# Kernel tuning notes

Measured on AMD Instinct MI355X. Metric: run time of the kernel, lower is better.

## Reference

```python
import jax, jax.numpy as jnp
import numpy as np

N = 50000   # nodes
R = 4       # relation groups
E = 800000  # nnz per relation adjacency
ED = 200000 # decoded edges
H = 128     # hidden_dim
L = 64      # latent_dim
DH = 64     # decoder_hidden_dim


def setup_inputs() -> dict:
    key = jax.random.key(0)
    ks = iter(jax.random.split(key, 64))
    def nrm(shape, scale=1.0):
        return jax.random.normal(next(ks), shape, dtype=jnp.float32) * scale
    inp = {}
    inp["x_process"] = nrm((N, 62))
    inp["x_file"] = nrm((N, 37))
    inp["x_network"] = nrm((N, 37))
    def lin(prefix, din, dout):
        s = 1.0 / np.sqrt(din)
        inp[prefix + "_Ws"] = nrm((dout, din), s)
        inp[prefix + "_bs"] = nrm((dout,), s)
        inp[prefix + "_Wr"] = nrm((R, dout, din), s)
        inp[prefix + "_br"] = nrm((R, dout), s)
    lin("p1", 62, H); lin("p2", H, L)
    lin("f1", 37, H); lin("f2", H, L)
    lin("n1", 37, H); lin("n2", H, L)
    inp["gate_W"] = nrm((3, L), 1.0 / np.sqrt(L))
    inp["gate_b"] = nrm((3,), 0.1)
    inp["dec_W1"] = nrm((DH, 4 * L), 1.0 / np.sqrt(4 * L))
    inp["dec_b1"] = nrm((DH,), 0.1)
    inp["dec_W2"] = nrm((1, DH), 1.0 / np.sqrt(DH))
    inp["dec_b2"] = nrm((1,), 0.1)
    inp["adj_rows"] = jax.random.randint(next(ks), (R, E), 0, N, dtype=jnp.int32)
    inp["adj_cols"] = jax.random.randint(next(ks), (R, E), 0, N, dtype=jnp.int32)
    inp["adj_vals"] = jax.random.uniform(next(ks), (R, E), dtype=jnp.float32) * 0.1
    inp["edge_src"] = jax.random.randint(next(ks), (ED,), 0, N, dtype=jnp.int32)
    inp["edge_dst"] = jax.random.randint(next(ks), (ED,), 0, N, dtype=jnp.int32)
    return inp


def reference(x_process, x_file, x_network,
              p1_Ws, p1_bs, p1_Wr, p1_br, p2_Ws, p2_bs, p2_Wr, p2_br,
              f1_Ws, f1_bs, f1_Wr, f1_br, f2_Ws, f2_bs, f2_Wr, f2_br,
              n1_Ws, n1_bs, n1_Wr, n1_br, n2_Ws, n2_bs, n2_Wr, n2_br,
              gate_W, gate_b, dec_W1, dec_b1, dec_W2, dec_b2,
              adj_rows, adj_cols, adj_vals, edge_src, edge_dst):
    def spmm(rows, cols, vals, x):  # A @ x, A in COO: out[row] += val * x[col]
        return jax.ops.segment_sum(vals[:, None] * x[cols], rows, num_segments=N)

    def rgcn_layer(x, Ws, bs, Wr, br):
        out = x @ Ws.T + bs  # self_linear
        for r in range(R):
            out = out + spmm(adj_rows[r], adj_cols[r], adj_vals[r], x) @ Wr[r].T + br[r]
        return out / float(R + 1)

    def encoder(x, W1s, b1s, W1r, b1r, W2s, b2s, W2r, b2r):
        h = jax.nn.relu(rgcn_layer(x, W1s, b1s, W1r, b1r))
        # dropout p=0.0 / eval mode -> identity
        return rgcn_layer(h, W2s, b2s, W2r, b2r)

    z_p = encoder(x_process, p1_Ws, p1_bs, p1_Wr, p1_br, p2_Ws, p2_bs, p2_Wr, p2_br)
    z_f = encoder(x_file, f1_Ws, f1_bs, f1_Wr, f1_br, f2_Ws, f2_bs, f2_Wr, f2_br)
    z_n = encoder(x_network, n1_Ws, n1_bs, n1_Wr, n1_br, n2_Ws, n2_bs, n2_Wr, n2_br)

    # gated multi-view fusion: three Linear(latent,1) gates -> softmax over views
    scores = jnp.stack([z_p @ gate_W[0] + gate_b[0],
                        z_f @ gate_W[1] + gate_b[1],
                        z_n @ gate_W[2] + gate_b[2]], axis=1)  # [N, 3]
    alpha = jax.nn.softmax(scores, axis=1)
    z = alpha[:, 0:1] * z_p + alpha[:, 1:2] * z_f + alpha[:, 2:3] * z_n  # [N, L]

    # mlp edge decoder
    zs = z[edge_src]
    zd = z[edge_dst]
    feats = jnp.concatenate([zs, zd, zs * zd, jnp.abs(zs - zd)], axis=1)  # [ED, 4L]
    hid = jax.nn.relu(feats @ dec_W1.T + dec_b1)
    logits = (hid @ dec_W2.T + dec_b2)[:, 0]  # [ED]
    return logits
```

## Files before the change

kernel.cpp:

```cpp
#include <hip/hip_runtime.h>

#define N_NODES 50000
#define R_REL   4
#define E_NNZ   800000
#define ED_EDGES 200000
#define H_DIM   128
#define L_DIM   64

#define RN_TOTAL (R_REL * N_NODES)
#define ETOT     (R_REL * E_NNZ)

#define EPB   8192
#define NB    391
#define RBK   196
#define KBK   (R_REL * RBK)
#define HTOT  (KBK * NB)
#define SCB   300
#define MAXB  6144

#define WS_RP    0u
#define WS_HIST  800256u
#define WS_BSUM  2026496u
#define WS_BIAS3 2028544u
#define WS_CV    2030592u
#define WS_YALL  27630720u
#define WS_TMP   27630720u
#define WS_UVZ   27630720u
#define WS_SF    53230720u
#define WS_SN    82830720u
#define WS_XALL  112430720u
#define WS_YSP   112430720u
#define WS_SP    131630720u
#define WS_HF    131630720u
#define WS_YSN   131630720u
#define WS_HN    157230720u
#define WS_HPR   188001536u
#define WS_YSF   188001536u
#define WS_Z     200801536u

__device__ __forceinline__ ushort f2bf(float f) {
    unsigned u = __float_as_uint(f);
    unsigned r = (u + 0x7fffu + ((u >> 16) & 1u)) >> 16;
    return (ushort)r;
}
__device__ __forceinline__ float bf2f(ushort u) {
    return __uint_as_float(((unsigned)u) << 16);
}

__global__ void cast_xall_kernel(const float* __restrict__ xp, const float* __restrict__ xf,
                                 const float* __restrict__ xn, ushort* __restrict__ xall) {
    int i = blockIdx.x * 256 + threadIdx.x;
    if (i >= N_NODES * 192) return;
    int node = i / 192, k = i - node * 192;
    float v = 0.f;
    if (k < 62) v = xp[node * 62 + k];
    else if (k >= 64 && k < 138) {
        int j = k - 64, d = j >> 1;
        v = (j & 1) ? xn[node * 37 + d] : xf[node * 37 + d];
    }
    xall[i] = f2bf(v);
}

__global__ void radix_hist_kernel(const int* __restrict__ rows, int* __restrict__ H) {
    __shared__ int hist[KBK];
    int blk = blockIdx.x, t = threadIdx.x;
    for (int i = t; i < KBK; i += 256) hist[i] = 0;
    __syncthreads();
    int base = blk * EPB;
    #pragma unroll 1
    for (int i = 0; i < EPB / 256; i++) {
        int g = base + i * 256 + t;
        if (g < ETOT) {
            int r = g / E_NNZ;
            atomicAdd(&hist[r * RBK + (rows[g] >> 8)], 1);
        }
    }
    __syncthreads();
    for (int i = t; i < KBK; i += 256) H[i * NB + blk] = hist[i];
}

__global__ void scan_part_kernel(const int* __restrict__ H, int* __restrict__ bsum) {
    __shared__ int red[256];
    int base = blockIdx.x * 1024, t = threadIdx.x;
    int s = 0;
    #pragma unroll
    for (int i = 0; i < 4; i++) {
        int idx = base + i * 256 + t;
        if (idx < HTOT) s += H[idx];
    }
    red[t] = s; __syncthreads();
    for (int d = 128; d > 0; d >>= 1) {
        if (t < d) red[t] += red[t + d];
        __syncthreads();
    }
    if (t == 0) bsum[blockIdx.x] = red[0];
}

__global__ void scan_bsum_kernel(int* __restrict__ bsum, int* __restrict__ rp) {
    __shared__ int sh[512];
    int t = threadIdx.x;
    int v = (t < SCB) ? bsum[t] : 0;
    sh[t] = v; __syncthreads();
    for (int d = 1; d < 512; d <<= 1) {
        int u = (t >= d) ? sh[t - d] : 0;
        __syncthreads();
        sh[t] += u;
        __syncthreads();
    }
    if (t < SCB) bsum[t] = sh[t] - v;
    if (t == 0) rp[RN_TOTAL] = ETOT;
}

__global__ void scan_final_kernel(int* __restrict__ H, const int* __restrict__ bsum) {
    __shared__ int sh[256];
    int base = blockIdx.x * 1024, t = threadIdx.x;
    int c[4]; int s = 0;
    #pragma unroll
    for (int i = 0; i < 4; i++) {
        int idx = base + t * 4 + i;
        c[i] = (idx < HTOT) ? H[idx] : 0;
        s += c[i];
    }
    sh[t] = s; __syncthreads();
    for (int d = 1; d < 256; d <<= 1) {
        int u = (t >= d) ? sh[t - d] : 0;
        __syncthreads();
        sh[t] += u;
        __syncthreads();
    }
    int off = bsum[blockIdx.x] + sh[t] - s;
    #pragma unroll
    for (int i = 0; i < 4; i++) {
        int idx = base + t * 4 + i;
        if (idx < HTOT) H[idx] = off;
        off += c[i];
    }
}

__global__ void radix_scatter_kernel(const int* __restrict__ rows, const int* __restrict__ cols,
                                     const float* __restrict__ vals, const int* __restrict__ H,
                                     int2* __restrict__ tmp) {
    __shared__ int cur[KBK];
    int blk = blockIdx.x, t = threadIdx.x;
    for (int i = t; i < KBK; i += 256) cur[i] = H[i * NB + blk];
    __syncthreads();
    int base = blk * EPB;
    #pragma unroll 1
    for (int i = 0; i < EPB / 256; i++) {
        int g = base + i * 256 + t;
        if (g < ETOT) {
            int r = g / E_NNZ;
            int row = rows[g];
            int b = r * RBK + (row >> 8);
            int p = atomicAdd(&cur[b], 1);
            tmp[p] = make_int2(cols[g] | ((row & 255) << 16), __float_as_int(vals[g]));
        }
    }
}

__launch_bounds__(256)
__global__ void bucket_sort_kernel(const int2* __restrict__ tmp, const int* __restrict__ H,
                                   int* __restrict__ rp, int2* __restrict__ cse) {
    __shared__ int hist[256];
    __shared__ int sc[256];
    __shared__ int cur[256];
    __shared__ int2 eb[MAXB];
    int b = blockIdx.x, t = threadIdx.x;
    int start = H[b * NB];
    int end = (b == KBK - 1) ? ETOT : H[(b + 1) * NB];
    int cnt = end - start;
    bool useLds = (cnt <= MAXB);
    hist[t] = 0;
    __syncthreads();
    for (int i = t; i < cnt; i += 256) {
        int2 e = tmp[start + i];
        if (useLds) eb[i] = e;
        atomicAdd(&hist[(e.x >> 16) & 255], 1);
    }
    __syncthreads();
    sc[t] = hist[t]; __syncthreads();
    for (int d = 1; d < 256; d <<= 1) {
        int v = (t >= d) ? sc[t - d] : 0;
        __syncthreads();
        sc[t] += v;
        __syncthreads();
    }
    int pref = sc[t] - hist[t];
    int r = b / RBK, rh = b - r * RBK;
    int grow = rh * 256 + t;
    if (grow < N_NODES) rp[r * N_NODES + grow] = start + pref;
    cur[t] = start + pref;
    __syncthreads();
    for (int i = t; i < cnt; i += 256) {
        int2 e = useLds ? eb[i] : tmp[start + i];
        int rl = (e.x >> 16) & 255;
        int p = atomicAdd(&cur[rl], 1);
        cse[p] = make_int2(e.x & 0xFFFF, e.y);
    }
}

__global__ void spmm1_all_kernel(const ushort* __restrict__ xall,
                                 const int* __restrict__ rp, const int2* __restrict__ cse,
                                 float* __restrict__ Sp, float* __restrict__ Sf,
                                 float* __restrict__ Sn) {
    int wave = threadIdx.x >> 6, lane = threadIdx.x & 63;
    int row = blockIdx.x * 4 + wave;
    if (row >= N_NODES) return;
    int h = lane >> 5, j = lane & 31;
    unsigned d0 = 2u * (unsigned)j;
    unsigned po = d0;
    unsigned fo = 64u + 2u * d0;
    for (int r = 0; r < R_REL; r++) {
        int e0 = rp[r * N_NODES + row], e1 = rp[r * N_NODES + row + 1];
        float ap0 = 0.f, ap1 = 0.f, af0 = 0.f, af1 = 0.f, an0 = 0.f, an1 = 0.f;
        int e = e0;
        for (; e + 8 <= e1; e += 8) {
            int2 qA = cse[e + h],     qB = cse[e + 2 + h];
            int2 qC = cse[e + 4 + h], qD = cse[e + 6 + h];
            unsigned bA = (unsigned)qA.x * 192u, bB = (unsigned)qB.x * 192u;
            unsigned bC = (unsigned)qC.x * 192u, bD = (unsigned)qD.x * 192u;
            ushort2 pA = *(const ushort2*)(xall + bA + po);
            ushort2 pB = *(const ushort2*)(xall + bB + po);
            ushort2 pC = *(const ushort2*)(xall + bC + po);
            ushort2 pD = *(const ushort2*)(xall + bD + po);
            ushort4 uA = *(const ushort4*)(xall + bA + fo);
            ushort4 uB = *(const ushort4*)(xall + bB + fo);
            ushort4 uC = *(const ushort4*)(xall + bC + fo);
            ushort4 uD = *(const ushort4*)(xall + bD + fo);
            float vA = __int_as_float(qA.y), vB = __int_as_float(qB.y);
            float vC = __int_as_float(qC.y), vD = __int_as_float(qD.y);
            ap0 += vA * bf2f(pA.x) + vB * bf2f(pB.x) + vC * bf2f(pC.x) + vD * bf2f(pD.x);
            ap1 += vA * bf2f(pA.y) + vB * bf2f(pB.y) + vC * bf2f(pC.y) + vD * bf2f(pD.y);
            af0 += vA * bf2f(uA.x) + vB * bf2f(uB.x) + vC * bf2f(uC.x) + vD * bf2f(uD.x);
            an0 += vA * bf2f(uA.y) + vB * bf2f(uB.y) + vC * bf2f(uC.y) + vD * bf2f(uD.y);
            af1 += vA * bf2f(uA.z) + vB * bf2f(uB.z) + vC * bf2f(uC.z) + vD * bf2f(uD.z);
            an1 += vA * bf2f(uA.w) + vB * bf2f(uB.w) + vC * bf2f(uC.w) + vD * bf2f(uD.w);
        }
        for (; e < e1; e += 2) {
            int idx = e + h;
            int2 q = cse[idx < e1 ? idx : e1 - 1];
            float v = (idx < e1) ? __int_as_float(q.y) : 0.f;
            unsigned b = (unsigned)q.x * 192u;
            ushort2 p = *(const ushort2*)(xall + b + po);
            ushort4 u = *(const ushort4*)(xall + b + fo);
            ap0 += v * bf2f(p.x); ap1 += v * bf2f(p.y);
            af0 += v * bf2f(u.x); an0 += v * bf2f(u.y);
            af1 += v * bf2f(u.z); an1 += v * bf2f(u.w);
        }
        ap0 += __shfl_xor(ap0, 32); ap1 += __shfl_xor(ap1, 32);
        af0 += __shfl_xor(af0, 32); af1 += __shfl_xor(af1, 32);
        an0 += __shfl_xor(an0, 32); an1 += __shfl_xor(an1, 32);
        if (h == 0) {
            int d = (int)d0;
            if (d < 62) *(float2*)(Sp + row * 248 + r * 62 + d) = make_float2(ap0, ap1);
            float* sfp = Sf + row * 148 + r * 37;
            float* snp = Sn + row * 148 + r * 37;
            if (d < 37) { sfp[d] = af0; snp[d] = an0; }
            if (d < 36) { sfp[d + 1] = af1; snp[d + 1] = an1; }
        }
    }
}

__launch_bounds__(256)
__global__ void gemm1_kernel(const float* __restrict__ x, const float* __restrict__ S,
                             const float* __restrict__ Ws, const float* __restrict__ bs,
                             const float* __restrict__ Wr, const float* __restrict__ br,
                             float* __restrict__ h, int din) {
    __shared__ float sA[64 * 63];
    __shared__ float sW[62 * 132];
    int t = threadIdx.x;
    int i0 = blockIdx.x * 64;
    int rg = t >> 5, cg = t & 31;
    float acc[8][4] = {};
    for (int s = 0; s < 5; s++) {
        const float* Aptr; int astride;
        if (s == 0) { Aptr = x; astride = din; }
        else        { Aptr = S + (s - 1) * din; astride = 4 * din; }
        const float* Wp = (s == 0) ? Ws : (Wr + (s - 1) * H_DIM * din);
        __syncthreads();
        for (int idx = t; idx < 64 * din; idx += 256) {
            int rr = idx / din, k = idx - rr * din;
            int grow = i0 + rr;
            sA[rr * 63 + k] = (grow < N_NODES) ? Aptr[grow * astride + k] : 0.f;
        }
        for (int idx = t; idx < H_DIM * din; idx += 256) {
            int j = idx / din, k = idx - j * din;
            sW[k * 132 + j] = Wp[j * din + k];
        }
        __syncthreads();
        for (int k = 0; k < din; k++) {
            float a[8];
            #pragma unroll
            for (int rr = 0; rr < 8; rr++) a[rr] = sA[(rg * 8 + rr) * 63 + k];
            float4 w = *(const float4*)&sW[k * 132 + cg * 4];
            #pragma unroll
            for (int rr = 0; rr < 8; rr++) {
                acc[rr][0] += a[rr] * w.x; acc[rr][1] += a[rr] * w.y;
                acc[rr][2] += a[rr] * w.z; acc[rr][3] += a[rr] * w.w;
            }
        }
    }
    int j0 = cg * 4;
    float btot[4];
    #pragma unroll
    for (int cc = 0; cc < 4; cc++) {
        float b = bs[j0 + cc];
        #pragma unroll
        for (int r = 0; r < R_REL; r++) b += br[r * H_DIM + j0 + cc];
        btot[cc] = b;
    }
    #pragma unroll
    for (int rr = 0; rr < 8; rr++) {
        int grow = i0 + rg * 8 + rr;
        if (grow < N_NODES) {
            float4 o;
            o.x = fmaxf((acc[rr][0] + btot[0]) * 0.2f, 0.f);
            o.y = fmaxf((acc[rr][1] + btot[1]) * 0.2f, 0.f);
            o.z = fmaxf((acc[rr][2] + btot[2]) * 0.2f, 0.f);
            o.w = fmaxf((acc[rr][3] + btot[3]) * 0.2f, 0.f);
            *(float4*)&h[grow * H_DIM + j0] = o;
        }
    }
}

__launch_bounds__(256)
__global__ void gemm2_kernel(const float* __restrict__ h, const float* __restrict__ Ws2,
                             const float* __restrict__ Wr2, float* __restrict__ Yself,
                             ushort* __restrict__ Yall, int view) {
    __shared__ float sA[128 * 65];
    __shared__ float sW[64 * 68];
    int t = threadIdx.x;
    int i0 = blockIdx.x * 128;
    int ct = blockIdx.y;
    int rg = t >> 4, cg = t & 15;
    const float* Wp = (ct == 0) ? Ws2 : (Wr2 + (ct - 1) * 64 * H_DIM);
    float acc[8][4] = {};
    for (int kc = 0; kc < 2; kc++) {
        __syncthreads();
        for (int idx = t; idx < 128 * 64; idx += 256) {
            int rr = idx >> 6, k = idx & 63;
            int grow = i0 + rr;
            sA[rr * 65 + k] = (grow < N_NODES) ? h[grow * H_DIM + kc * 64 + k] : 0.f;
        }
        for (int idx = t; idx < 64 * 64; idx += 256) {
            int j = idx >> 6, k = idx & 63;
            sW[k * 68 + j] = Wp[j * H_DIM + kc * 64 + k];
        }
        __syncthreads();
        for (int k = 0; k < 64; k++) {
            float a[8];
            #pragma unroll
            for (int rr = 0; rr < 8; rr++) a[rr] = sA[(rg * 8 + rr) * 65 + k];
            float4 w = *(const float4*)&sW[k * 68 + cg * 4];
            #pragma unroll
            for (int rr = 0; rr < 8; rr++) {
                acc[rr][0] += a[rr] * w.x; acc[rr][1] += a[rr] * w.y;
                acc[rr][2] += a[rr] * w.z; acc[rr][3] += a[rr] * w.w;
            }
        }
    }
    #pragma unroll
    for (int rr = 0; rr < 8; rr++) {
        int grow = i0 + rg * 8 + rr;
        if (grow < N_NODES) {
            if (ct == 0) {
                float4 o = make_float4(acc[rr][0], acc[rr][1], acc[rr][2], acc[rr][3]);
                *(float4*)&Yself[(size_t)grow * 64 + cg * 4] = o;
            } else {
                ushort4 o;
                o.x = f2bf(acc[rr][0]); o.y = f2bf(acc[rr][1]);
                o.z = f2bf(acc[rr][2]); o.w = f2bf(acc[rr][3]);
                *(ushort4*)&Yall[(size_t)grow * 768 + (ct - 1) * 192 + view * 64 + cg * 4] = o;
            }
        }
    }
}

__global__ void bias_prep_kernel(const float* __restrict__ pbs, const float* __restrict__ pbr,
                                 const float* __restrict__ fbs, const float* __restrict__ fbr,
                                 const float* __restrict__ nbs, const float* __restrict__ nbr,
                                 float* __restrict__ bias3) {
    int t = threadIdx.x;
    if (t >= 192) return;
    int view = t >> 6, d = t & 63;
    const float* bs = (view == 0) ? pbs : (view == 1) ? fbs : nbs;
    const float* br = (view == 0) ? pbr : (view == 1) ? fbr : nbr;
    float b = bs[d];
    #pragma unroll
    for (int r = 0; r < R_REL; r++) b += br[r * 64 + d];
    bias3[t] = b;
}

__launch_bounds__(256)
__global__ void spmm2z_all_kernel(const float* __restrict__ Ysp,
                                  const float* __restrict__ Ysf,
                                  const float* __restrict__ Ysn,
                                  const ushort* __restrict__ Yall,
                                  const int* __restrict__ rp, const int2* __restrict__ cse,
                                  const float* __restrict__ bias3,
                                  const float* __restrict__ gW, const float* __restrict__ gb,
                                  float* __restrict__ z) {
    int wave = threadIdx.x >> 6, lane = threadIdx.x & 63;
    int row = blockIdx.x * 4 + wave;
    if (row >= N_NODES) return;
    int h = lane >> 5, j = lane & 31;
    unsigned d0 = 2u * (unsigned)j;
    float aP0 = 0.f, aP1 = 0.f, aF0 = 0.f, aF1 = 0.f, aN0 = 0.f, aN1 = 0.f;
    for (int r = 0; r < R_REL; r++) {
        int e0 = rp[r * N_NODES + row], e1 = rp[r * N_NODES + row + 1];
        unsigned ofs = (unsigned)(r * 192) + d0;
        int e = e0;
        for (; e + 8 <= e1; e += 8) {
            int2 qA = cse[e + h],     qB = cse[e + 2 + h];
            int2 qC = cse[e + 4 + h], qD = cse[e + 6 + h];
            unsigned oA = (unsigned)qA.x * 768u + ofs;
            unsigned oB = (unsigned)qB.x * 768u + ofs;
            unsigned oC = (unsigned)qC.x * 768u + ofs;
            unsigned oD = (unsigned)qD.x * 768u + ofs;
            ushort2 pA = *(const ushort2*)(Yall + oA);
            ushort2 fA = *(const ushort2*)(Yall + oA + 64);
            ushort2 nA = *(const ushort2*)(Yall + oA + 128);
            ushort2 pB = *(const ushort2*)(Yall + oB);
            ushort2 fB = *(const ushort2*)(Yall + oB + 64);
            ushort2 nB = *(const ushort2*)(Yall + oB + 128);
            ushort2 pC = *(const ushort2*)(Yall + oC);
            ushort2 fC = *(const ushort2*)(Yall + oC + 64);
            ushort2 nC = *(const ushort2*)(Yall + oC + 128);
            ushort2 pD = *(const ushort2*)(Yall + oD);
            ushort2 fD = *(const ushort2*)(Yall + oD + 64);
            ushort2 nD = *(const ushort2*)(Yall + oD + 128);
            float vA = __int_as_float(qA.y), vB = __int_as_float(qB.y);
            float vC = __int_as_float(qC.y), vD = __int_as_float(qD.y);
            aP0 += vA * bf2f(pA.x) + vB * bf2f(pB.x) + vC * bf2f(pC.x) + vD * bf2f(pD.x);
            aP1 += vA * bf2f(pA.y) + vB * bf2f(pB.y) + vC * bf2f(pC.y) + vD * bf2f(pD.y);
            aF0 += vA * bf2f(fA.x) + vB * bf2f(fB.x) + vC * bf2f(fC.x) + vD * bf2f(fD.x);
            aF1 += vA * bf2f(fA.y) + vB * bf2f(fB.y) + vC * bf2f(fC.y) + vD * bf2f(fD.y);
            aN0 += vA * bf2f(nA.x) + vB * bf2f(nB.x) + vC * bf2f(nC.x) + vD * bf2f(nD.x);
            aN1 += vA * bf2f(nA.y) + vB * bf2f(nB.y) + vC * bf2f(nC.y) + vD * bf2f(nD.y);
        }
        for (; e < e1; e += 2) {
            int idx = e + h;
            int2 q = cse[idx < e1 ? idx : e1 - 1];
            float v = (idx < e1) ? __int_as_float(q.y) : 0.f;
            unsigned o = (unsigned)q.x * 768u + ofs;
            ushort2 p = *(const ushort2*)(Yall + o);
            ushort2 f = *(const ushort2*)(Yall + o + 64);
            ushort2 n = *(const ushort2*)(Yall + o + 128);
            aP0 += v * bf2f(p.x); aP1 += v * bf2f(p.y);
            aF0 += v * bf2f(f.x); aF1 += v * bf2f(f.y);
            aN0 += v * bf2f(n.x); aN1 += v * bf2f(n.y);
        }
    }
    aP0 += __shfl_xor(aP0, 32); aP1 += __shfl_xor(aP1, 32);
    aF0 += __shfl_xor(aF0, 32); aF1 += __shfl_xor(aF1, 32);
    aN0 += __shfl_xor(aN0, 32); aN1 += __shfl_xor(aN1, 32);
    size_t rb = (size_t)row * 64 + d0;
    float2 ysp = *(const float2*)(Ysp + rb);
    float2 ysf = *(const float2*)(Ysf + rb);
    float2 ysn = *(const float2*)(Ysn + rb);
    aP0 = (aP0 + ysp.x + bias3[d0]) * 0.2f;
    aP1 = (aP1 + ysp.y + bias3[d0 + 1]) * 0.2f;
    aF0 = (aF0 + ysf.x + bias3[64 + d0]) * 0.2f;
    aF1 = (aF1 + ysf.y + bias3[64 + d0 + 1]) * 0.2f;
    aN0 = (aN0 + ysn.x + bias3[128 + d0]) * 0.2f;
    aN1 = (aN1 + ysn.y + bias3[128 + d0 + 1]) * 0.2f;
    float sp = aP0 * gW[d0] + aP1 * gW[d0 + 1];
    float sf = aF0 * gW[64 + d0] + aF1 * gW[64 + d0 + 1];
    float sn = aN0 * gW[128 + d0] + aN1 * gW[128 + d0 + 1];
    #pragma unroll
    for (int d = 16; d >= 1; d >>= 1) {
        sp += __shfl_xor(sp, d);
        sf += __shfl_xor(sf, d);
        sn += __shfl_xor(sn, d);
    }
    sp += gb[0]; sf += gb[1]; sn += gb[2];
    float m = fmaxf(sp, fmaxf(sf, sn));
    float ep = __expf(sp - m), ef = __expf(sf - m), en = __expf(sn - m);
    float inv = 1.f / (ep + ef + en);
    if (h == 0) {
        float2 zo;
        zo.x = (ep * aP0 + ef * aF0 + en * aN0) * inv;
        zo.y = (ep * aP1 + ef * aF1 + en * aN1) * inv;
        *(float2*)(z + rb) = zo;
    }
}

__launch_bounds__(256)
__global__ void uvgemm_kernel(const float* __restrict__ z, const float* __restrict__ w1,
                              const float* __restrict__ b1, float* __restrict__ uvz) {
    __shared__ float sA[128 * 65];
    __shared__ float sW[64 * 68];
    int t = threadIdx.x;
    int i0 = blockIdx.x * 128;
    int ct = blockIdx.y;
    int rg = t >> 4, cg = t & 15;
    for (int idx = t; idx < 128 * 64; idx += 256) {
        int rr = idx >> 6, k = idx & 63;
        int grow = i0 + rr;
        sA[rr * 65 + k] = (grow < N_NODES) ? z[(size_t)grow * 64 + k] : 0.f;
    }
    for (int idx = t; idx < 64 * 64; idx += 256) {
        int j = idx >> 6, k = idx & 63;
        sW[k * 68 + j] = w1[j * 256 + ct * 64 + k];
    }
    __syncthreads();
    float acc[8][4] = {};
    for (int k = 0; k < 64; k++) {
        float a[8];
        #pragma unroll
        for (int rr = 0; rr < 8; rr++) a[rr] = sA[(rg * 8 + rr) * 65 + k];
        float4 w = *(const float4*)&sW[k * 68 + cg * 4];
        #pragma unroll
        for (int rr = 0; rr < 8; rr++) {
            acc[rr][0] += a[rr] * w.x; acc[rr][1] += a[rr] * w.y;
            acc[rr][2] += a[rr] * w.z; acc[rr][3] += a[rr] * w.w;
        }
    }
    int j0 = cg * 4;
    float4 bv = make_float4(0.f, 0.f, 0.f, 0.f);
    if (ct == 0) {
        bv.x = b1[j0]; bv.y = b1[j0 + 1]; bv.z = b1[j0 + 2]; bv.w = b1[j0 + 3];
    }
    unsigned voff = (ct == 0) ? 0u : 128u;
    #pragma unroll
    for (int rr = 0; rr < 8; rr++) {
        int grow = i0 + rg * 8 + rr;
        if (grow < N_NODES) {
            float4 o = make_float4(acc[rr][0] + bv.x, acc[rr][1] + bv.y,
                                   acc[rr][2] + bv.z, acc[rr][3] + bv.w);
            *(float4*)&uvz[(size_t)grow * 192 + voff + j0] = o;
        }
    }
    if (ct == 0) {
        for (int idx = t; idx < 128 * 64; idx += 256) {
            int rr = idx >> 6, k = idx & 63;
            int grow = i0 + rr;
            if (grow < N_NODES) uvz[(size_t)grow * 192 + 64 + k] = sA[rr * 65 + k];
        }
    }
}

__launch_bounds__(256)
__global__ void decoder9_kernel(const float* __restrict__ uvz, const int* __restrict__ esrc,
                                const int* __restrict__ edst, const float* __restrict__ w1,
                                const float* __restrict__ w2, const float* __restrict__ b2,
                                float* __restrict__ out) {
    __shared__ float sW1[8192];
    int t = threadIdx.x;
    for (int i = t; i < 2048; i += 256) {
        int j = i >> 5, c = i & 31;
        ((float4*)sW1)[i] = *(const float4*)(w1 + j * 256 + 128 + c * 4);
    }
    __syncthreads();
    int e = blockIdx.x * 256 + t;
    if (e >= ED_EDGES) return;
    int s = esrc[e], d = edst[e];
    const float4* su = (const float4*)(uvz + (size_t)s * 192);
    const float4* dv = (const float4*)(uvz + (size_t)d * 192 + 64);
    float hid[64];
    #pragma unroll
    for (int j = 0; j < 64; j++) hid[j] = 0.f;
    #pragma unroll 1
    for (int kc = 0; kc < 16; kc++) {
        float4 a = su[16 + kc];
        float4 b = dv[kc];
        float4 p, q;
        p.x = a.x * b.x; q.x = fabsf(a.x - b.x);
        p.y = a.y * b.y; q.y = fabsf(a.y - b.y);
        p.z = a.z * b.z; q.z = fabsf(a.z - b.z);
        p.w = a.w * b.w; q.w = fabsf(a.w - b.w);
        const float* wb0 = sW1 + kc * 4;
        #pragma unroll
        for (int j = 0; j < 64; j++) {
            const float* wr = wb0 + j * 128;
            float4 wc = *(const float4*)(wr);
            float4 wd = *(const float4*)(wr + 64);
            hid[j] += p.x * wc.x + p.y * wc.y + p.z * wc.z + p.w * wc.w
                    + q.x * wd.x + q.y * wd.y + q.z * wd.z + q.w * wd.w;
        }
    }
    float lg = b2[0];
    #pragma unroll
    for (int jj = 0; jj < 16; jj++) {
        float4 u = su[jj];
        float4 v = dv[16 + jj];
        int gj = jj * 4;
        float w0 = w2[gj], w1v = w2[gj + 1], w2v = w2[gj + 2], w3v = w2[gj + 3];
        lg += fmaxf(hid[gj]     + u.x + v.x, 0.f) * w0
            + fmaxf(hid[gj + 1] + u.y + v.y, 0.f) * w1v
            + fmaxf(hid[gj + 2] + u.z + v.z, 0.f) * w2v
            + fmaxf(hid[gj + 3] + u.w + v.w, 0.f) * w3v;
    }
    out[e] = lg;
}

extern "C" void kernel_launch(void* const* d_in, const int* in_sizes, int n_in,
                              void* d_out, int out_size, void* d_ws, size_t ws_size,
                              hipStream_t stream) {
    const float* x_p = (const float*)d_in[0];
    const float* x_f = (const float*)d_in[1];
    const float* x_n = (const float*)d_in[2];
    const float* p1_Ws = (const float*)d_in[3];  const float* p1_bs = (const float*)d_in[4];
    const float* p1_Wr = (const float*)d_in[5];  const float* p1_br = (const float*)d_in[6];
    const float* p2_Ws = (const float*)d_in[7];  const float* p2_bs = (const float*)d_in[8];
    const float* p2_Wr = (const float*)d_in[9];  const float* p2_br = (const float*)d_in[10];
    const float* f1_Ws = (const float*)d_in[11]; const float* f1_bs = (const float*)d_in[12];
    const float* f1_Wr = (const float*)d_in[13]; const float* f1_br = (const float*)d_in[14];
    const float* f2_Ws = (const float*)d_in[15]; const float* f2_bs = (const float*)d_in[16];
    const float* f2_Wr = (const float*)d_in[17]; const float* f2_br = (const float*)d_in[18];
    const float* n1_Ws = (const float*)d_in[19]; const float* n1_bs = (const float*)d_in[20];
    const float* n1_Wr = (const float*)d_in[21]; const float* n1_br = (const float*)d_in[22];
    const float* n2_Ws = (const float*)d_in[23]; const float* n2_bs = (const float*)d_in[24];
    const float* n2_Wr = (const float*)d_in[25]; const float* n2_br = (const float*)d_in[26];
    const float* gate_W = (const float*)d_in[27]; const float* gate_b = (const float*)d_in[28];
    const float* dec_W1 = (const float*)d_in[29]; const float* dec_b1 = (const float*)d_in[30];
    const float* dec_W2 = (const float*)d_in[31]; const float* dec_b2 = (const float*)d_in[32];
    const int*   adj_rows = (const int*)d_in[33];
    const int*   adj_cols = (const int*)d_in[34];
    const float* adj_vals = (const float*)d_in[35];
    const int*   edge_src = (const int*)d_in[36];
    const int*   edge_dst = (const int*)d_in[37];

    char* ws = (char*)d_ws;
    int*    rp   = (int*)(ws + WS_RP);
    int*    H    = (int*)(ws + WS_HIST);
    int*    bsum = (int*)(ws + WS_BSUM);
    float*  bias3 = (float*)(ws + WS_BIAS3);
    int2*   cse  = (int2*)(ws + WS_CV);
    int2*   tmp  = (int2*)(ws + WS_TMP);
    ushort* xall = (ushort*)(ws + WS_XALL);
    ushort* Yall = (ushort*)(ws + WS_YALL);
    float*  S_p = (float*)(ws + WS_SP);
    float*  S_f = (float*)(ws + WS_SF);
    float*  S_n = (float*)(ws + WS_SN);
    float*  h_p = (float*)(ws + WS_HPR);
    float*  h_f = (float*)(ws + WS_HF);
    float*  h_n = (float*)(ws + WS_HN);
    float*  Ys_p = (float*)(ws + WS_YSP);
    float*  Ys_f = (float*)(ws + WS_YSF);
    float*  Ys_n = (float*)(ws + WS_YSN);
    float*  z    = (float*)(ws + WS_Z);
    float*  uvz  = (float*)(ws + WS_UVZ);
    float*  out  = (float*)d_out;

    cast_xall_kernel<<<(N_NODES * 192 + 255) / 256, 256, 0, stream>>>(x_p, x_f, x_n, xall);

    radix_hist_kernel<<<NB, 256, 0, stream>>>(adj_rows, H);
    scan_part_kernel<<<SCB, 256, 0, stream>>>(H, bsum);
    scan_bsum_kernel<<<1, 512, 0, stream>>>(bsum, rp);
    scan_final_kernel<<<SCB, 256, 0, stream>>>(H, bsum);
    radix_scatter_kernel<<<NB, 256, 0, stream>>>(adj_rows, adj_cols, adj_vals, H, tmp);
    bucket_sort_kernel<<<KBK, 256, 0, stream>>>(tmp, H, rp, cse);

    spmm1_all_kernel<<<N_NODES / 4, 256, 0, stream>>>(xall, rp, cse, S_p, S_f, S_n);

    int g1 = (N_NODES + 63) / 64;
    gemm1_kernel<<<g1, 256, 0, stream>>>(x_p, S_p, p1_Ws, p1_bs, p1_Wr, p1_br, h_p, 62);
    gemm1_kernel<<<g1, 256, 0, stream>>>(x_f, S_f, f1_Ws, f1_bs, f1_Wr, f1_br, h_f, 37);
    gemm1_kernel<<<g1, 256, 0, stream>>>(x_n, S_n, n1_Ws, n1_bs, n1_Wr, n1_br, h_n, 37);

    dim3 g2((N_NODES + 127) / 128, 5);
    gemm2_kernel<<<g2, 256, 0, stream>>>(h_p, p2_Ws, p2_Wr, Ys_p, Yall, 0);
    gemm2_kernel<<<g2, 256, 0, stream>>>(h_f, f2_Ws, f2_Wr, Ys_f, Yall, 1);
    gemm2_kernel<<<g2, 256, 0, stream>>>(h_n, n2_Ws, n2_Wr, Ys_n, Yall, 2);

    bias_prep_kernel<<<1, 192, 0, stream>>>(p2_bs, p2_br, f2_bs, f2_br, n2_bs, n2_br, bias3);
    spmm2z_all_kernel<<<N_NODES / 4, 256, 0, stream>>>(
        Ys_p, Ys_f, Ys_n, Yall, rp, cse, bias3, gate_W, gate_b, z);

    dim3 guv((N_NODES + 127) / 128, 2);
    uvgemm_kernel<<<guv, 256, 0, stream>>>(z, dec_W1, dec_b1, uvz);

    decoder9_kernel<<<(ED_EDGES + 255) / 256, 256, 0, stream>>>(
        uvz, edge_src, edge_dst, dec_W1, dec_W2, dec_b2, out);
}
```

Before: 1.381 ms.

## Replace two-pass radix CSR build with atomic count-scan-scatter; transpose GEMM A tiles

```diff
diff --git a/kernel.cpp b/kernel.cpp
--- a/kernel.cpp
+++ b/kernel.cpp
@@ -10,13 +10,7 @@
 #define RN_TOTAL (R_REL * N_NODES)
 #define ETOT     (R_REL * E_NNZ)
 
-#define EPB   8192
-#define NB    391
-#define RBK   196
-#define KBK   (R_REL * RBK)
-#define HTOT  (KBK * NB)
-#define SCB   300
-#define MAXB  6144
+#define SCB2  196
 
 #define WS_RP    0u
 #define WS_HIST  800256u
@@ -24,7 +18,6 @@
 #define WS_BIAS3 2028544u
 #define WS_CV    2030592u
 #define WS_YALL  27630720u
-#define WS_TMP   27630720u
 #define WS_UVZ   27630720u
 #define WS_SF    53230720u
 #define WS_SN    82830720u
@@ -61,32 +54,27 @@
     xall[i] = f2bf(v);
 }
 
-__global__ void radix_hist_kernel(const int* __restrict__ rows, int* __restrict__ H) {
-    __shared__ int hist[KBK];
-    int blk = blockIdx.x, t = threadIdx.x;
-    for (int i = t; i < KBK; i += 256) hist[i] = 0;
-    __syncthreads();
-    int base = blk * EPB;
-    #pragma unroll 1
-    for (int i = 0; i < EPB / 256; i++) {
-        int g = base + i * 256 + t;
-        if (g < ETOT) {
-            int r = g / E_NNZ;
-            atomicAdd(&hist[r * RBK + (rows[g] >> 8)], 1);
-        }
-    }
-    __syncthreads();
-    for (int i = t; i < KBK; i += 256) H[i * NB + blk] = hist[i];
-}
-
-__global__ void scan_part_kernel(const int* __restrict__ H, int* __restrict__ bsum) {
+__global__ void zero_cnt_kernel(int* __restrict__ cnt) {
+    int i = blockIdx.x * 256 + threadIdx.x;
+    if (i < RN_TOTAL) cnt[i] = 0;
+}
+
+__global__ void row_hist_kernel(const int* __restrict__ rows, int* __restrict__ cnt) {
+    int g = blockIdx.x * 256 + threadIdx.x;
+    if (g < ETOT) {
+        int r = g / E_NNZ;
+        atomicAdd(&cnt[r * N_NODES + rows[g]], 1);
+    }
+}
+
+__global__ void scan_part_kernel(const int* __restrict__ cnt, int* __restrict__ bsum) {
     __shared__ int red[256];
     int base = blockIdx.x * 1024, t = threadIdx.x;
     int s = 0;
     #pragma unroll
     for (int i = 0; i < 4; i++) {
         int idx = base + i * 256 + t;
-        if (idx < HTOT) s += H[idx];
+        if (idx < RN_TOTAL) s += cnt[idx];
     }
     red[t] = s; __syncthreads();
     for (int d = 128; d > 0; d >>= 1) {
@@ -99,7 +87,7 @@
 __global__ void scan_bsum_kernel(int* __restrict__ bsum, int* __restrict__ rp) {
     __shared__ int sh[512];
     int t = threadIdx.x;
-    int v = (t < SCB) ? bsum[t] : 0;
+    int v = (t < SCB2) ? bsum[t] : 0;
     sh[t] = v; __syncthreads();
     for (int d = 1; d < 512; d <<= 1) {
         int u = (t >= d) ? sh[t - d] : 0;
@@ -107,18 +95,19 @@
         sh[t] += u;
         __syncthreads();
     }
-    if (t < SCB) bsum[t] = sh[t] - v;
+    if (t < SCB2) bsum[t] = sh[t] - v;
     if (t == 0) rp[RN_TOTAL] = ETOT;
 }
 
-__global__ void scan_final_kernel(int* __restrict__ H, const int* __restrict__ bsum) {
+__global__ void scan_final_kernel(int* __restrict__ cnt, const int* __restrict__ bsum,
+                                  int* __restrict__ rp) {
     __shared__ int sh[256];
     int base = blockIdx.x * 1024, t = threadIdx.x;
     int c[4]; int s = 0;
     #pragma unroll
     for (int i = 0; i < 4; i++) {
         int idx = base + t * 4 + i;
-        c[i] = (idx < HTOT) ? H[idx] : 0;
+        c[i] = (idx < RN_TOTAL) ? cnt[idx] : 0;
         s += c[i];
     }
     sh[t] = s; __syncthreads();
@@ -132,70 +121,19 @@
     #pragma unroll
     for (int i = 0; i < 4; i++) {
         int idx = base + t * 4 + i;
-        if (idx < HTOT) H[idx] = off;
+        if (idx < RN_TOTAL) { rp[idx] = off; cnt[idx] = off; }
         off += c[i];
     }
 }
 
-__global__ void radix_scatter_kernel(const int* __restrict__ rows, const int* __restrict__ cols,
-                                     const float* __restrict__ vals, const int* __restrict__ H,
-                                     int2* __restrict__ tmp) {
-    __shared__ int cur[KBK];
-    int blk = blockIdx.x, t = threadIdx.x;
-    for (int i = t; i < KBK; i += 256) cur[i] = H[i * NB + blk];
-    __syncthreads();
-    int base = blk * EPB;
-    #pragma unroll 1
-    for (int i = 0; i < EPB / 256; i++) {
-        int g = base + i * 256 + t;
-        if (g < ETOT) {
-            int r = g / E_NNZ;
-            int row = rows[g];
-            int b = r * RBK + (row >> 8);
-            int p = atomicAdd(&cur[b], 1);
-            tmp[p] = make_int2(cols[g] | ((row & 255) << 16), __float_as_int(vals[g]));
-        }
-    }
-}
-
-__launch_bounds__(256)
-__global__ void bucket_sort_kernel(const int2* __restrict__ tmp, const int* __restrict__ H,
-                                   int* __restrict__ rp, int2* __restrict__ cse) {
-    __shared__ int hist[256];
-    __shared__ int sc[256];
-    __shared__ int cur[256];
-    __shared__ int2 eb[MAXB];
-    int b = blockIdx.x, t = threadIdx.x;
-    int start = H[b * NB];
-    int end = (b == KBK - 1) ? ETOT : H[(b + 1) * NB];
-    int cnt = end - start;
-    bool useLds = (cnt <= MAXB);
-    hist[t] = 0;
-    __syncthreads();
-    for (int i = t; i < cnt; i += 256) {
-        int2 e = tmp[start + i];
-        if (useLds) eb[i] = e;
-        atomicAdd(&hist[(e.x >> 16) & 255], 1);
-    }
-    __syncthreads();
-    sc[t] = hist[t]; __syncthreads();
-    for (int d = 1; d < 256; d <<= 1) {
-        int v = (t >= d) ? sc[t - d] : 0;
-        __syncthreads();
-        sc[t] += v;
-        __syncthreads();
-    }
-    int pref = sc[t] - hist[t];
-    int r = b / RBK, rh = b - r * RBK;
-    int grow = rh * 256 + t;
-    if (grow < N_NODES) rp[r * N_NODES + grow] = start + pref;
-    cur[t] = start + pref;
-    __syncthreads();
-    for (int i = t; i < cnt; i += 256) {
-        int2 e = useLds ? eb[i] : tmp[start + i];
-        int rl = (e.x >> 16) & 255;
-        int p = atomicAdd(&cur[rl], 1);
-        cse[p] = make_int2(e.x & 0xFFFF, e.y);
+__global__ void scatter_direct_kernel(const int* __restrict__ rows, const int* __restrict__ cols,
+                                      const float* __restrict__ vals, int* __restrict__ cur,
+                                      int2* __restrict__ cse) {
+    int g = blockIdx.x * 256 + threadIdx.x;
+    if (g < ETOT) {
+        int r = g / E_NNZ;
+        int p = atomicAdd(&cur[r * N_NODES + rows[g]], 1);
+        cse[p] = make_int2(cols[g], __float_as_int(vals[g]));
     }
 }
 
@@ -266,7 +204,7 @@
                              const float* __restrict__ Ws, const float* __restrict__ bs,
                              const float* __restrict__ Wr, const float* __restrict__ br,
                              float* __restrict__ h, int din) {
-    __shared__ float sA[64 * 63];
+    __shared__ float sAT[62 * 68];
     __shared__ float sW[62 * 132];
     int t = threadIdx.x;
     int i0 = blockIdx.x * 64;
@@ -281,7 +219,7 @@
         for (int idx = t; idx < 64 * din; idx += 256) {
             int rr = idx / din, k = idx - rr * din;
             int grow = i0 + rr;
-            sA[rr * 63 + k] = (grow < N_NODES) ? Aptr[grow * astride + k] : 0.f;
+            sAT[k * 68 + rr] = (grow < N_NODES) ? Aptr[grow * astride + k] : 0.f;
         }
         for (int idx = t; idx < H_DIM * din; idx += 256) {
             int j = idx / din, k = idx - j * din;
@@ -289,9 +227,9 @@
         }
         __syncthreads();
         for (int k = 0; k < din; k++) {
-            float a[8];
-            #pragma unroll
-            for (int rr = 0; rr < 8; rr++) a[rr] = sA[(rg * 8 + rr) * 63 + k];
+            float4 a01 = *(const float4*)&sAT[k * 68 + rg * 8];
+            float4 a45 = *(const float4*)&sAT[k * 68 + rg * 8 + 4];
+            float a[8] = {a01.x, a01.y, a01.z, a01.w, a45.x, a45.y, a45.z, a45.w};
             float4 w = *(const float4*)&sW[k * 132 + cg * 4];
             #pragma unroll
             for (int rr = 0; rr < 8; rr++) {
@@ -327,7 +265,7 @@
 __global__ void gemm2_kernel(const float* __restrict__ h, const float* __restrict__ Ws2,
                              const float* __restrict__ Wr2, float* __restrict__ Yself,
                              ushort* __restrict__ Yall, int view) {
-    __shared__ float sA[128 * 65];
+    __shared__ float sAT[64 * 136];
     __shared__ float sW[64 * 68];
     int t = threadIdx.x;
     int i0 = blockIdx.x * 128;
@@ -340,7 +278,7 @@
         for (int idx = t; idx < 128 * 64; idx += 256) {
             int rr = idx >> 6, k = idx & 63;
             int grow = i0 + rr;
-            sA[rr * 65 + k] = (grow < N_NODES) ? h[grow * H_DIM + kc * 64 + k] : 0.f;
+            sAT[k * 136 + rr] = (grow < N_NODES) ? h[grow * H_DIM + kc * 64 + k] : 0.f;
         }
         for (int idx = t; idx < 64 * 64; idx += 256) {
             int j = idx >> 6, k = idx & 63;
@@ -348,9 +286,9 @@
         }
         __syncthreads();
         for (int k = 0; k < 64; k++) {
-            float a[8];
-            #pragma unroll
-            for (int rr = 0; rr < 8; rr++) a[rr] = sA[(rg * 8 + rr) * 65 + k];
+            float4 a01 = *(const float4*)&sAT[k * 136 + rg * 8];
+            float4 a45 = *(const float4*)&sAT[k * 136 + rg * 8 + 4];
+            float a[8] = {a01.x, a01.y, a01.z, a01.w, a45.x, a45.y, a45.z, a45.w};
             float4 w = *(const float4*)&sW[k * 68 + cg * 4];
             #pragma unroll
             for (int rr = 0; rr < 8; rr++) {
@@ -488,7 +426,7 @@
 __launch_bounds__(256)
 __global__ void uvgemm_kernel(const float* __restrict__ z, const float* __restrict__ w1,
                               const float* __restrict__ b1, float* __restrict__ uvz) {
-    __shared__ float sA[128 * 65];
+    __shared__ float sAT[64 * 136];
     __shared__ float sW[64 * 68];
     int t = threadIdx.x;
     int i0 = blockIdx.x * 128;
@@ -497,7 +435,7 @@
     for (int idx = t; idx < 128 * 64; idx += 256) {
         int rr = idx >> 6, k = idx & 63;
         int grow = i0 + rr;
-        sA[rr * 65 + k] = (grow < N_NODES) ? z[(size_t)grow * 64 + k] : 0.f;
+        sAT[k * 136 + rr] = (grow < N_NODES) ? z[(size_t)grow * 64 + k] : 0.f;
     }
     for (int idx = t; idx < 64 * 64; idx += 256) {
         int j = idx >> 6, k = idx & 63;
@@ -506,9 +444,9 @@
     __syncthreads();
     float acc[8][4] = {};
     for (int k = 0; k < 64; k++) {
-        float a[8];
-        #pragma unroll
-        for (int rr = 0; rr < 8; rr++) a[rr] = sA[(rg * 8 + rr) * 65 + k];
+        float4 a01 = *(const float4*)&sAT[k * 136 + rg * 8];
+        float4 a45 = *(const float4*)&sAT[k * 136 + rg * 8 + 4];
+        float a[8] = {a01.x, a01.y, a01.z, a01.w, a45.x, a45.y, a45.z, a45.w};
         float4 w = *(const float4*)&sW[k * 68 + cg * 4];
         #pragma unroll
         for (int rr = 0; rr < 8; rr++) {
@@ -535,7 +473,7 @@
         for (int idx = t; idx < 128 * 64; idx += 256) {
             int rr = idx >> 6, k = idx & 63;
             int grow = i0 + rr;
-            if (grow < N_NODES) uvz[(size_t)grow * 192 + 64 + k] = sA[rr * 65 + k];
+            if (grow < N_NODES) uvz[(size_t)grow * 192 + 64 + k] = sAT[k * 136 + rr];
         }
     }
 }
@@ -623,11 +561,10 @@
 
     char* ws = (char*)d_ws;
     int*    rp   = (int*)(ws + WS_RP);
-    int*    H    = (int*)(ws + WS_HIST);
+    int*    cnt  = (int*)(ws + WS_HIST);
     int*    bsum = (int*)(ws + WS_BSUM);
     float*  bias3 = (float*)(ws + WS_BIAS3);
     int2*   cse  = (int2*)(ws + WS_CV);
-    int2*   tmp  = (int2*)(ws + WS_TMP);
     ushort* xall = (ushort*)(ws + WS_XALL);
     ushort* Yall = (ushort*)(ws + WS_YALL);
     float*  S_p = (float*)(ws + WS_SP);
@@ -645,12 +582,13 @@
 
     cast_xall_kernel<<<(N_NODES * 192 + 255) / 256, 256, 0, stream>>>(x_p, x_f, x_n, xall);
 
-    radix_hist_kernel<<<NB, 256, 0, stream>>>(adj_rows, H);
-    scan_part_kernel<<<SCB, 256, 0, stream>>>(H, bsum);
+    zero_cnt_kernel<<<(RN_TOTAL + 255) / 256, 256, 0, stream>>>(cnt);
+    row_hist_kernel<<<(ETOT + 255) / 256, 256, 0, stream>>>(adj_rows, cnt);
+    scan_part_kernel<<<SCB2, 256, 0, stream>>>(cnt, bsum);
     scan_bsum_kernel<<<1, 512, 0, stream>>>(bsum, rp);
-    scan_final_kernel<<<SCB, 256, 0, stream>>>(H, bsum);
-    radix_scatter_kernel<<<NB, 256, 0, stream>>>(adj_rows, adj_cols, adj_vals, H, tmp);
-    bucket_sort_kernel<<<KBK, 256, 0, stream>>>(tmp, H, rp, cse);
+    scan_final_kernel<<<SCB2, 256, 0, stream>>>(cnt, bsum, rp);
+    scatter_direct_kernel<<<(ETOT + 255) / 256, 256, 0, stream>>>(
+        adj_rows, adj_cols, adj_vals, cnt, cse);
 
     spmm1_all_kernel<<<N_NODES / 4, 256, 0, stream>>>(xall, rp, cse, S_p, S_f, S_n);
 
```

New measurement: 1.579 ms. 14.4% more time.
